# Performance work log

Hardware: AMD Instinct MI355X
Metric: run time of the kernel (lower is better)

Reference implementation:

```python
import jax, jax.numpy as jnp
import numpy as np

N = 50000          # nodes
E = 1_600_000      # edges (avg degree 32)
IN_CH = 256
HID = 256          # 2 * out_channels
OUT_CH = 128


def setup_inputs() -> dict:
    key = jax.random.key(0)
    k = jax.random.split(key, 5)
    x = jax.random.normal(k[0], (N, IN_CH), dtype=jnp.float32)
    edge_index = jax.random.randint(k[1], (2, E), 0, N, dtype=jnp.int64)
    W1 = jax.random.normal(k[2], (IN_CH, HID), dtype=jnp.float32) * 0.05
    b1 = jnp.zeros((HID,), dtype=jnp.float32)
    W2 = jax.random.normal(k[3], (HID, OUT_CH), dtype=jnp.float32) * 0.05
    b2 = jnp.zeros((OUT_CH,), dtype=jnp.float32)
    return {"x": x, "edge_index": edge_index, "W1": W1, "b1": b1, "W2": W2, "b2": b2}


def _gcn_conv(x, src, dst, deg_inv_sqrt, W, b, n_nodes):
    # GCNConv: linear transform, then normalized sum-aggregation over edges
    # (edge list already includes self-loops; deg_inv_sqrt precomputed).
    h = x @ W                                   # [N, F_out]
    norm = deg_inv_sqrt[src] * deg_inv_sqrt[dst]  # [E+N]
    msg = h[src] * norm[:, None]                # gather + scale
    out = jax.ops.segment_sum(msg, dst, num_segments=n_nodes)  # scatter-add
    return out + b


def reference(x, edge_index, W1, b1, W2, b2):
    n = x.shape[0]
    loop = jnp.arange(n, dtype=edge_index.dtype)
    src = jnp.concatenate([edge_index[0], loop])   # with self-loops
    dst = jnp.concatenate([edge_index[1], loop])
    # symmetric degree normalization (edge weight 1, deg over targets)
    deg = jax.ops.segment_sum(jnp.ones_like(dst, dtype=x.dtype), dst, num_segments=n)
    deg_inv_sqrt = jnp.where(deg > 0, jax.lax.rsqrt(deg), 0.0)

    z = _gcn_conv(x, src, dst, deg_inv_sqrt, W1, b1, n)
    z = jax.nn.relu(z)
    z = _gcn_conv(z, src, dst, deg_inv_sqrt, W2, b2, n)

    # decode: gather endpoint embeddings of original edges, dot product
    value = jnp.sum(z[edge_index[0]] * z[edge_index[1]], axis=-1)  # [E]
    return value.reshape(-1)
```

## Files before the change

### kernel.cpp

```cpp
#include <hip/hip_runtime.h>

#define WS_ALIGN(x) (((x) + 255) & ~(size_t)255)

typedef float f4v __attribute__((ext_vector_type(4)));
typedef __attribute__((ext_vector_type(8))) short bf16x8;
typedef __attribute__((ext_vector_type(4))) float f32x4;
typedef __attribute__((ext_vector_type(4))) unsigned short us4;

__device__ inline void nt_store4(float* p, float4 v) {
  __builtin_nontemporal_store(*(f4v*)&v, (f4v*)p);
}

__device__ inline unsigned short f2bf(float v) {
  unsigned int u = __float_as_uint(v);
  u += 0x7FFF + ((u >> 16) & 1);
  return (unsigned short)(u >> 16);
}
__device__ inline float bf2f(unsigned short h) {
  return __uint_as_float(((unsigned int)h) << 16);
}

__global__ void k_pack_count(const int* __restrict__ src, const int* __restrict__ dst, int E,
                             unsigned int* __restrict__ packed, int* __restrict__ deg) {
  int e = blockIdx.x * blockDim.x + threadIdx.x;
  if (e < E) {
    int s = src[e];
    int d = dst[e];
    packed[e] = (unsigned int)s | ((unsigned int)d << 16);
    atomicAdd(&deg[d], 1);
  }
}

__global__ void k_dis(const int* __restrict__ deg, float* __restrict__ dis, int N) {
  int i = blockIdx.x * blockDim.x + threadIdx.x;
  if (i < N) dis[i] = rsqrtf((float)(deg[i] + 1));
}

__global__ __launch_bounds__(1024) void k_scan(const int* __restrict__ deg,
                                               int* __restrict__ rowptr,
                                               int* __restrict__ cursor,
                                               int N, int Etot) {
  __shared__ int wsum[16];
  __shared__ int s_carry;
  int tid = threadIdx.x, lane = tid & 63, w = tid >> 6;
  if (tid == 0) { s_carry = 0; rowptr[N] = Etot; }
  __syncthreads();
  for (int base = 0; base < N; base += 4096) {
    int i0 = base + tid * 4;
    int v[4];
    #pragma unroll
    for (int u = 0; u < 4; ++u) {
      int i = i0 + u;
      v[u] = (i < N) ? deg[i] : 0;
    }
    int tsum = v[0] + v[1] + v[2] + v[3];
    int sc = tsum;
    #pragma unroll
    for (int off = 1; off < 64; off <<= 1) {
      int t = __shfl_up(sc, off);
      if (lane >= off) sc += t;
    }
    if (lane == 63) wsum[w] = sc;
    __syncthreads();
    if (w == 0 && lane < 16) {
      int xx = wsum[lane];
      #pragma unroll
      for (int off = 1; off < 16; off <<= 1) {
        int t = __shfl_up(xx, off);
        if (lane >= off) xx += t;
      }
      wsum[lane] = xx;
    }
    __syncthreads();
    int woff = (w == 0) ? 0 : wsum[w - 1];
    int excl = s_carry + woff + (sc - tsum);
    #pragma unroll
    for (int u = 0; u < 4; ++u) {
      int i = i0 + u;
      if (i < N) { rowptr[i] = excl; cursor[i] = excl; }
      excl += v[u];
    }
    __syncthreads();
    if (tid == 0) s_carry += wsum[15];
    __syncthreads();
  }
}

__global__ __launch_bounds__(256) void k_fill_xcd(const unsigned int* __restrict__ packed,
                                                  int E, int N,
                                                  int* __restrict__ cursor,
                                                  unsigned short* __restrict__ csr16) {
  int bid = blockIdx.x;
  int xcd = bid & 7;
  int tix = ((bid >> 3) << 8) + threadIdx.x;
  int tpx = ((int)(gridDim.x >> 3)) << 8;
  int lo = (int)(((long long)N * xcd) >> 3);
  int hi = (int)(((long long)N * (xcd + 1)) >> 3);
  for (int e = tix; e < E; e += tpx) {
    unsigned int pk = packed[e];
    int d = (int)(pk >> 16);
    if (d >= lo && d < hi) {
      int pos = atomicAdd(&cursor[d], 1);
      csr16[pos] = (unsigned short)(pk & 0xFFFFu);
    }
  }
}

#define APAD 40
__global__ __launch_bounds__(256) void k_gemm_mfma_sm(const float* __restrict__ A,
                                                      const float* __restrict__ B,
                                                      const float* __restrict__ dis,
                                                      float* __restrict__ C,
                                                      int M, int Nc, int K) {
  __shared__ unsigned short As_hi[128][APAD];
  __shared__ unsigned short As_lo[128][APAD];
  __shared__ unsigned short Bs_hi[64][APAD];
  __shared__ unsigned short Bs_lo[64][APAD];
  int tid = threadIdx.x;
  int wv = tid >> 6, lane = tid & 63;
  int block_row = blockIdx.x * 128;
  int block_col = blockIdx.y * 64;

  f32x4 acc[2][4] = {};

  for (int k0 = 0; k0 < K; k0 += 32) {
    {
      int row = tid >> 1;
      int grow = block_row + row;
      int qb = (tid & 1) * 16;
      const float* ap = A + (size_t)grow * K + k0 + qb;
      #pragma unroll
      for (int i = 0; i < 4; ++i) {
        float4 v = {0.f, 0.f, 0.f, 0.f};
        if (grow < M) v = *(const float4*)(ap + i * 4);
        us4 h, l;
        h.x = f2bf(v.x); h.y = f2bf(v.y); h.z = f2bf(v.z); h.w = f2bf(v.w);
        l.x = f2bf(v.x - bf2f(h.x)); l.y = f2bf(v.y - bf2f(h.y));
        l.z = f2bf(v.z - bf2f(h.z)); l.w = f2bf(v.w - bf2f(h.w));
        *(us4*)&As_hi[row][qb + i * 4] = h;
        *(us4*)&As_lo[row][qb + i * 4] = l;
      }
    }
    {
      int n = tid & 63;
      int ksb = (tid >> 6) * 8;
      int gn = block_col + n;
      #pragma unroll
      for (int j = 0; j < 8; ++j) {
        float v = B[(size_t)(k0 + ksb + j) * Nc + gn];
        unsigned short h = f2bf(v);
        Bs_hi[n][ksb + j] = h;
        Bs_lo[n][ksb + j] = f2bf(v - bf2f(h));
      }
    }
    __syncthreads();
    int frow = lane & 15;
    int fk = (lane >> 4) * 8;
    bf16x8 ah[2], al[2], bh[4], bl[4];
    #pragma unroll
    for (int rf = 0; rf < 2; ++rf) {
      int r = wv * 32 + rf * 16 + frow;
      ah[rf] = *(const bf16x8*)&As_hi[r][fk];
      al[rf] = *(const bf16x8*)&As_lo[r][fk];
    }
    #pragma unroll
    for (int cf = 0; cf < 4; ++cf) {
      int c = cf * 16 + frow;
      bh[cf] = *(const bf16x8*)&Bs_hi[c][fk];
      bl[cf] = *(const bf16x8*)&Bs_lo[c][fk];
    }
    #pragma unroll
    for (int rf = 0; rf < 2; ++rf)
      #pragma unroll
      for (int cf = 0; cf < 4; ++cf) {
        acc[rf][cf] = __builtin_amdgcn_mfma_f32_16x16x32_bf16(ah[rf], bh[cf], acc[rf][cf], 0, 0, 0);
        acc[rf][cf] = __builtin_amdgcn_mfma_f32_16x16x32_bf16(ah[rf], bl[cf], acc[rf][cf], 0, 0, 0);
        acc[rf][cf] = __builtin_amdgcn_mfma_f32_16x16x32_bf16(al[rf], bh[cf], acc[rf][cf], 0, 0, 0);
      }
    __syncthreads();
  }
  int fcol = lane & 15;
  #pragma unroll
  for (int rf = 0; rf < 2; ++rf) {
    int rbase = block_row + wv * 32 + rf * 16 + (lane >> 4) * 4;
    #pragma unroll
    for (int j = 0; j < 4; ++j) {
      int row = rbase + j;
      if (row < M) {
        float dn = dis[row];
        #pragma unroll
        for (int cf = 0; cf < 4; ++cf) {
          int sl = (block_col >> 4) + cf;
          C[((size_t)sl * M + row) * 16 + fcol] = acc[rf][cf][j] * dn;
        }
      }
    }
  }
}

template <int FCH, bool OUTSLICE>
__global__ __launch_bounds__(256) void k_agg_xcd(const float* __restrict__ hs,
                                                 const int* __restrict__ rowptr,
                                                 const unsigned short* __restrict__ csr,
                                                 const float* __restrict__ dis,
                                                 const float* __restrict__ bias,
                                                 float* __restrict__ out,
                                                 int N, int do_relu, int phase) {
  int bid = blockIdx.x;
  int xcd = bid & 7;
  int wid = threadIdx.x >> 6;
  int lane = threadIdx.x & 63;
  int sub = lane >> 3;
  int epar = (lane >> 2) & 1;
  int c2 = lane & 3;
  int wix = ((bid >> 3) << 2) + wid;
  int wpx = ((int)(gridDim.x >> 3)) << 2;
  int nchunk = (N + 7) >> 3;

  int s = xcd + (phase << 3);
  const float* in = hs + (size_t)s * N * 16;
  for (int ch = wix; ch < nchunk; ch += wpx) {
    int node = (ch << 3) + sub;
    bool valid = node < N;
    int b0 = 0, e0 = 0;
    if (valid) { b0 = rowptr[node]; e0 = rowptr[node + 1]; }
    float4 acc = {0.f, 0.f, 0.f, 0.f};
    int j = b0 + epar;
    for (; j + 6 < e0; j += 8) {
      int i0 = csr[j];     int i1 = csr[j + 2];
      int i2 = csr[j + 4]; int i3 = csr[j + 6];
      float4 v0 = *(const float4*)(in + ((size_t)i0 << 4) + (c2 << 2));
      float4 v1 = *(const float4*)(in + ((size_t)i1 << 4) + (c2 << 2));
      float4 v2 = *(const float4*)(in + ((size_t)i2 << 4) + (c2 << 2));
      float4 v3 = *(const float4*)(in + ((size_t)i3 << 4) + (c2 << 2));
      acc.x += (v0.x + v1.x) + (v2.x + v3.x);
      acc.y += (v0.y + v1.y) + (v2.y + v3.y);
      acc.z += (v0.z + v1.z) + (v2.z + v3.z);
      acc.w += (v0.w + v1.w) + (v2.w + v3.w);
    }
    for (; j < e0; j += 2) {
      int idx = csr[j];
      float4 v = *(const float4*)(in + ((size_t)idx << 4) + (c2 << 2));
      acc.x += v.x; acc.y += v.y; acc.z += v.z; acc.w += v.w;
    }
    acc.x += __shfl_xor(acc.x, 4);
    acc.y += __shfl_xor(acc.y, 4);
    acc.z += __shfl_xor(acc.z, 4);
    acc.w += __shfl_xor(acc.w, 4);
    if (valid && epar == 0) {
      float4 self = *(const float4*)(in + ((size_t)node << 4) + (c2 << 2));
      float dn = dis[node];
      int col = (s << 4) + (c2 << 2);
      float4 bv = *(const float4*)(bias + col);
      float4 r;
      r.x = (acc.x + self.x) * dn + bv.x;
      r.y = (acc.y + self.y) * dn + bv.y;
      r.z = (acc.z + self.z) * dn + bv.z;
      r.w = (acc.w + self.w) * dn + bv.w;
      if (do_relu) {
        r.x = fmaxf(r.x, 0.f); r.y = fmaxf(r.y, 0.f);
        r.z = fmaxf(r.z, 0.f); r.w = fmaxf(r.w, 0.f);
      }
      if (OUTSLICE)
        nt_store4(out + (size_t)s * N * 16 + ((size_t)node << 4) + (c2 << 2), r);
      else
        nt_store4(out + (size_t)node * FCH + col, r);
    }
  }
}

__global__ __launch_bounds__(256) void k_decode_xcd4(const float* __restrict__ z,
                                                     const unsigned int* __restrict__ packed,
                                                     float* __restrict__ partial,
                                                     int E, int N) {
  int bid = blockIdx.x;
  int xcd = bid & 7;
  int wid = threadIdx.x >> 6;
  int lane = threadIdx.x & 63;
  int c2 = lane & 3;
  int sub = lane >> 2;
  int wix = ((bid >> 3) << 2) + wid;
  int wpx = ((int)(gridDim.x >> 3)) << 2;
  const float* zc = z + (size_t)xcd * N * 16;
  float* pp = partial + (size_t)xcd * E;

  for (int e0 = wix * 64; e0 < E; e0 += wpx * 64) {
    float pv[4];
    int ev[4];
    #pragma unroll
    for (int q = 0; q < 4; ++q) {
      int e = e0 + q * 16 + sub;
      ev[q] = e;
      pv[q] = 0.f;
      if (e < E) {
        unsigned int pk = packed[e];
        int a = (int)(pk & 0xFFFFu), d = (int)(pk >> 16);
        float4 za = *(const float4*)(zc + ((size_t)a << 4) + (c2 << 2));
        float4 zb = *(const float4*)(zc + ((size_t)d << 4) + (c2 << 2));
        pv[q] = za.x * zb.x + za.y * zb.y + za.z * zb.z + za.w * zb.w;
      }
    }
    #pragma unroll
    for (int q = 0; q < 4; ++q) {
      pv[q] += __shfl_xor(pv[q], 1);
      pv[q] += __shfl_xor(pv[q], 2);
    }
    if (c2 == 0) {
      #pragma unroll
      for (int q = 0; q < 4; ++q)
        if (ev[q] < E) pp[ev[q]] = pv[q];
    }
  }
}

__global__ void k_dreduce4(const float* __restrict__ partial, float* __restrict__ out, int E) {
  int q = blockIdx.x * 256 + threadIdx.x;
  int e = q << 2;
  if (e >= E) return;
  if (e + 4 <= E) {
    float4 s = *(const float4*)(partial + e);
    #pragma unroll
    for (int k = 1; k < 8; ++k) {
      float4 t = *(const float4*)(partial + (size_t)k * E + e);
      s.x += t.x; s.y += t.y; s.z += t.z; s.w += t.w;
    }
    *(float4*)(out + e) = s;
  } else {
    for (int i = e; i < E; ++i) {
      float s = 0.f;
      #pragma unroll
      for (int k = 0; k < 8; ++k) s += partial[(size_t)k * E + i];
      out[i] = s;
    }
  }
}

extern "C" void kernel_launch(void* const* d_in, const int* in_sizes, int n_in,
                              void* d_out, int out_size, void* d_ws, size_t ws_size,
                              hipStream_t stream) {
  const float* x  = (const float*)d_in[0];
  const int* eidx = (const int*)d_in[1];
  const float* W1 = (const float*)d_in[2];
  const float* b1 = (const float*)d_in[3];
  const float* W2 = (const float*)d_in[4];
  const float* b2 = (const float*)d_in[5];
  float* out = (float*)d_out;

  const int IN_CH = 256, HID = 256, OUT_CH = 128;
  const int N = in_sizes[0] / IN_CH;
  const int E = in_sizes[1] / 2;
  const int* esrc = eidx;
  const int* edst = eidx + E;

  char* p = (char*)d_ws;
  auto alloc = [&](size_t bytes) -> char* { char* r = p; p += WS_ALIGN(bytes); return r; };
  int*   deg    = (int*)  alloc(sizeof(int) * N);
  float* dis    = (float*)alloc(sizeof(float) * N);
  int*   rowptr = (int*)  alloc(sizeof(int) * (N + 1));
  int*   cursor = (int*)  alloc(sizeof(int) * N);
  unsigned short* csr16 = (unsigned short*)alloc(sizeof(unsigned short) * (size_t)E);
  unsigned int*   packed = (unsigned int*) alloc(sizeof(unsigned int) * (size_t)E);
  float* bufA   = (float*)alloc(sizeof(float) * (size_t)N * HID);
  float* bufB   = (float*)alloc(sizeof(float) * (size_t)N * HID);

  const int T = 256;
  const int PG = 2048;

  hipMemsetAsync(deg, 0, sizeof(int) * N, stream);
  hipLaunchKernelGGL(k_pack_count, dim3((E + T - 1) / T), dim3(T), 0, stream,
                     esrc, edst, E, packed, deg);
  hipLaunchKernelGGL(k_dis, dim3((N + T - 1) / T), dim3(T), 0, stream, deg, dis, N);
  hipLaunchKernelGGL(k_scan, dim3(1), dim3(1024), 0, stream, deg, rowptr, cursor, N, E);
  hipLaunchKernelGGL(k_fill_xcd, dim3(PG), dim3(T), 0, stream, packed, E, N, cursor, csr16);

  dim3 g1((N + 127) / 128, HID / 64);
  hipLaunchKernelGGL(k_gemm_mfma_sm, g1, dim3(256), 0, stream, x, W1, dis, bufA, N, HID, IN_CH);
  hipLaunchKernelGGL((k_agg_xcd<256, false>), dim3(PG), dim3(256), 0, stream,
                     bufA, rowptr, csr16, dis, b1, bufB, N, 1, 0);
  hipLaunchKernelGGL((k_agg_xcd<256, false>), dim3(PG), dim3(256), 0, stream,
                     bufA, rowptr, csr16, dis, b1, bufB, N, 1, 1);

  dim3 g2((N + 127) / 128, OUT_CH / 64);
  hipLaunchKernelGGL(k_gemm_mfma_sm, g2, dim3(256), 0, stream, bufB, W2, dis, bufA, N, OUT_CH, HID);
  hipLaunchKernelGGL((k_agg_xcd<128, true>), dim3(PG), dim3(256), 0, stream,
                     bufA, rowptr, csr16, dis, b2, bufB, N, 0, 0);

  hipLaunchKernelGGL(k_decode_xcd4, dim3(PG), dim3(256), 0, stream,
                     bufB, packed, bufA, E, N);
  hipLaunchKernelGGL(k_dreduce4, dim3((E / 4 + 255) / 256), dim3(256), 0, stream,
                     bufA, out, E);
}
```

Baseline: 626.6 us.

## Process aggregation nodes in degree-sorted order for wave load balance

Builds a degree-bucketed node permutation using a histogram, a bin scan and an atomic scatter, then has each aggregation wave handle 8 nodes of similar degree through that permutation. The aim is to reduce lane divergence, since lanes working on high-degree nodes otherwise stall lanes with short edge lists. It adds three small kernels, a memset and an extra indirection load. Output writes now land on scattered node rows, which loses write locality, and the atomic scatter makes node order within a bin nondeterministic.

```diff
diff --git a/kernel.cpp b/kernel.cpp
--- a/kernel.cpp
+++ b/kernel.cpp
@@ -34,6 +34,36 @@
 __global__ void k_dis(const int* __restrict__ deg, float* __restrict__ dis, int N) {
   int i = blockIdx.x * blockDim.x + threadIdx.x;
   if (i < N) dis[i] = rsqrtf((float)(deg[i] + 1));
+}
+
+__global__ void k_hist(const int* __restrict__ deg, int N, int* __restrict__ hist) {
+  int i = blockIdx.x * blockDim.x + threadIdx.x;
+  if (i < N) atomicAdd(&hist[min(deg[i], 255)], 1);
+}
+
+__global__ __launch_bounds__(256) void k_scan_bins(const int* __restrict__ hist,
+                                                   int* __restrict__ bin_cur) {
+  __shared__ int buf[256];
+  int t = threadIdx.x;
+  buf[t] = hist[t];
+  __syncthreads();
+  for (int off = 1; off < 256; off <<= 1) {
+    int v = (t >= off) ? buf[t - off] : 0;
+    __syncthreads();
+    buf[t] += v;
+    __syncthreads();
+  }
+  bin_cur[t] = (t == 0) ? 0 : buf[t - 1];
+}
+
+__global__ void k_scatter_perm(const int* __restrict__ deg, int N,
+                               int* __restrict__ bin_cur, unsigned short* __restrict__ perm) {
+  int i = blockIdx.x * blockDim.x + threadIdx.x;
+  if (i < N) {
+    int b = min(deg[i], 255);
+    int pos = atomicAdd(&bin_cur[b], 1);
+    perm[pos] = (unsigned short)i;
+  }
 }
 
 __global__ __launch_bounds__(1024) void k_scan(const int* __restrict__ deg,
@@ -202,6 +232,7 @@
 __global__ __launch_bounds__(256) void k_agg_xcd(const float* __restrict__ hs,
                                                  const int* __restrict__ rowptr,
                                                  const unsigned short* __restrict__ csr,
+                                                 const unsigned short* __restrict__ perm,
                                                  const float* __restrict__ dis,
                                                  const float* __restrict__ bias,
                                                  float* __restrict__ out,
@@ -220,10 +251,15 @@
   int s = xcd + (phase << 3);
   const float* in = hs + (size_t)s * N * 16;
   for (int ch = wix; ch < nchunk; ch += wpx) {
-    int node = (ch << 3) + sub;
-    bool valid = node < N;
+    int pidx = (ch << 3) + sub;
+    bool valid = pidx < N;
+    int node = 0;
     int b0 = 0, e0 = 0;
-    if (valid) { b0 = rowptr[node]; e0 = rowptr[node + 1]; }
+    if (valid) {
+      node = perm[pidx];
+      b0 = rowptr[node];
+      e0 = rowptr[node + 1];
+    }
     float4 acc = {0.f, 0.f, 0.f, 0.f};
     int j = b0 + epar;
     for (; j + 6 < e0; j += 8) {
@@ -358,6 +394,9 @@
   float* dis    = (float*)alloc(sizeof(float) * N);
   int*   rowptr = (int*)  alloc(sizeof(int) * (N + 1));
   int*   cursor = (int*)  alloc(sizeof(int) * N);
+  int*   hist   = (int*)  alloc(sizeof(int) * 256);
+  int*   bin_cur= (int*)  alloc(sizeof(int) * 256);
+  unsigned short* perm  = (unsigned short*)alloc(sizeof(unsigned short) * N);
   unsigned short* csr16 = (unsigned short*)alloc(sizeof(unsigned short) * (size_t)E);
   unsigned int*   packed = (unsigned int*) alloc(sizeof(unsigned int) * (size_t)E);
   float* bufA   = (float*)alloc(sizeof(float) * (size_t)N * HID);
@@ -367,23 +406,28 @@
   const int PG = 2048;
 
   hipMemsetAsync(deg, 0, sizeof(int) * N, stream);
+  hipMemsetAsync(hist, 0, sizeof(int) * 256, stream);
   hipLaunchKernelGGL(k_pack_count, dim3((E + T - 1) / T), dim3(T), 0, stream,
                      esrc, edst, E, packed, deg);
   hipLaunchKernelGGL(k_dis, dim3((N + T - 1) / T), dim3(T), 0, stream, deg, dis, N);
+  hipLaunchKernelGGL(k_hist, dim3((N + T - 1) / T), dim3(T), 0, stream, deg, N, hist);
+  hipLaunchKernelGGL(k_scan_bins, dim3(1), dim3(256), 0, stream, hist, bin_cur);
+  hipLaunchKernelGGL(k_scatter_perm, dim3((N + T - 1) / T), dim3(T), 0, stream,
+                     deg, N, bin_cur, perm);
   hipLaunchKernelGGL(k_scan, dim3(1), dim3(1024), 0, stream, deg, rowptr, cursor, N, E);
   hipLaunchKernelGGL(k_fill_xcd, dim3(PG), dim3(T), 0, stream, packed, E, N, cursor, csr16);
 
   dim3 g1((N + 127) / 128, HID / 64);
   hipLaunchKernelGGL(k_gemm_mfma_sm, g1, dim3(256), 0, stream, x, W1, dis, bufA, N, HID, IN_CH);
   hipLaunchKernelGGL((k_agg_xcd<256, false>), dim3(PG), dim3(256), 0, stream,
-                     bufA, rowptr, csr16, dis, b1, bufB, N, 1, 0);
+                     bufA, rowptr, csr16, perm, dis, b1, bufB, N, 1, 0);
   hipLaunchKernelGGL((k_agg_xcd<256, false>), dim3(PG), dim3(256), 0, stream,
-                     bufA, rowptr, csr16, dis, b1, bufB, N, 1, 1);
+                     bufA, rowptr, csr16, perm, dis, b1, bufB, N, 1, 1);
 
   dim3 g2((N + 127) / 128, OUT_CH / 64);
   hipLaunchKernelGGL(k_gemm_mfma_sm, g2, dim3(256), 0, stream, bufB, W2, dis, bufA, N, OUT_CH, HID);
   hipLaunchKernelGGL((k_agg_xcd<128, true>), dim3(PG), dim3(256), 0, stream,
-                     bufA, rowptr, csr16, dis, b2, bufB, N, 0, 0);
+                     bufA, rowptr, csr16, perm, dis, b2, bufB, N, 0, 0);
 
   hipLaunchKernelGGL(k_decode_xcd4, dim3(PG), dim3(256), 0, stream,
                      bufB, packed, bufA, E, N);
```

Result: slower. 873.3 us (+39.4%).
